# Optimization experiments

Measured on AMD Instinct MI355X. Metric: run time of the kernel, lower is better.

Reference implementation:

```python
import jax, jax.numpy as jnp
import numpy as np

N = 50000      # nodes
E = 800000     # edges (before self-loops)
DIN = 146      # input feature dim
D = 128        # hidden/out dim
G = 64         # graphs in batch
L = 4          # number of GCNConv layers (len(hidden_dims[1:]) + 1)
NC = 10        # classes
EPS = 1e-5     # BatchNorm eps


def setup_inputs() -> dict:
    key = jax.random.key(0)
    ks = jax.random.split(key, 12)
    x = jax.random.normal(ks[0], (N, DIN), jnp.float32)
    edge_index = jax.random.randint(ks[1], (2, E), 0, N, dtype=jnp.int64)
    batch = jnp.sort(jax.random.randint(ks[2], (N,), 0, G, dtype=jnp.int64))

    def lin(k, shape, fan_in):
        return (jax.random.normal(k, shape, jnp.float32) / np.sqrt(fan_in)).astype(jnp.float32)

    W_emb = lin(ks[3], (DIN, D), DIN)
    b_emb = jnp.zeros((D,), jnp.float32)
    W_gcn = lin(ks[4], (L, D, D), D)
    b_gcn = jnp.zeros((L, D), jnp.float32)
    bn_gamma = jnp.ones((L, D), jnp.float32)
    bn_beta = jnp.zeros((L, D), jnp.float32)
    W_r1 = lin(ks[5], (D, D // 2), D)
    b_r1 = jnp.zeros((D // 2,), jnp.float32)
    W_r2 = lin(ks[6], (D // 2, D // 4), D // 2)
    b_r2 = jnp.zeros((D // 4,), jnp.float32)
    W_r3 = lin(ks[7], (D // 4, NC), D // 4)
    b_r3 = jnp.zeros((NC,), jnp.float32)
    return {"x": x, "edge_index": edge_index, "batch": batch,
            "W_emb": W_emb, "b_emb": b_emb, "W_gcn": W_gcn, "b_gcn": b_gcn,
            "bn_gamma": bn_gamma, "bn_beta": bn_beta,
            "W_r1": W_r1, "b_r1": b_r1, "W_r2": W_r2, "b_r2": b_r2,
            "W_r3": W_r3, "b_r3": b_r3}


def reference(x, edge_index, batch, W_emb, b_emb, W_gcn, b_gcn,
              bn_gamma, bn_beta, W_r1, b_r1, W_r2, b_r2, W_r3, b_r3):
    # gcn_norm with self-loops (fill_value=1, improved=False)
    loop = jnp.arange(N, dtype=edge_index.dtype)
    src = jnp.concatenate([edge_index[0], loop])
    dst = jnp.concatenate([edge_index[1], loop])
    deg = jax.ops.segment_sum(jnp.ones(src.shape, x.dtype), dst, num_segments=N)
    dinv = jax.lax.rsqrt(jnp.maximum(deg, jnp.asarray(1e-12, x.dtype)))  # deg >= 1 (self loops)
    norm = (dinv[src] * dinv[dst])[:, None]  # [E+N, 1]

    h = x @ W_emb + b_emb  # embedding_h
    for l in range(L):
        h_in = h
        m = h @ W_gcn[l]                                            # [N, D]
        h = jax.ops.segment_sum(m[src] * norm, dst, num_segments=N) + b_gcn[l]
        # BatchNorm1d (training-mode batch stats, biased var)
        mu = h.mean(axis=0)
        var = h.var(axis=0)
        h = (h - mu) * jax.lax.rsqrt(var + EPS) * bn_gamma[l] + bn_beta[l]
        h = jax.nn.relu(h)
        h = h_in + h  # residual (dims always match here)

    # global_mean_pool over batch ids
    sums = jax.ops.segment_sum(h, batch, num_segments=G)
    cnts = jax.ops.segment_sum(jnp.ones((N, 1), h.dtype), batch, num_segments=G)
    hg = sums / jnp.maximum(cnts, 1.0)

    # MLPReadout: two hidden layers halving dims, then classifier
    z = jax.nn.relu(hg @ W_r1 + b_r1)
    z = jax.nn.relu(z @ W_r2 + b_r2)
    return z @ W_r3 + b_r3  # [G, NC]
```

## Files before the change

kernel.cpp:

```cpp
#include <hip/hip_runtime.h>
#include <hip/hip_bf16.h>

#define NN 50000
#define EE 800000
#define DIN 146
#define DD 128
#define GG 64
#define LL 4
#define NC 10
#define BN_EPS 1e-5f

#define KP_EMB 160
#define AST_L  136
#define NCOPY 64
#define NPW 4

typedef __attribute__((ext_vector_type(8))) short bf16x8;
typedef __attribute__((ext_vector_type(4))) float f32x4;

__device__ __forceinline__ float bf2f(__hip_bfloat16 v) { return __bfloat162float(v); }
__device__ __forceinline__ float loadf(const void* p, long i, int f32) {
    return f32 ? ((const float*)p)[i] : bf2f(((const __hip_bfloat16*)p)[i]);
}
__device__ __forceinline__ unsigned short f2bf_bits(float f) {
    __hip_bfloat16 h = __float2bfloat16(f);
    return *(unsigned short*)&h;
}
__device__ __forceinline__ float bfu2f(unsigned short u) {
    return __uint_as_float((unsigned)u << 16);
}

__global__ void detect_kernel(const void* ei, const void* batch, const void* Wemb,
                              int* __restrict__ flags) {
    __shared__ int s_edge_nz, s_batch_nz, s_f32_cnt;
    int t = threadIdx.x;
    if (t == 0) { s_edge_nz = 0; s_batch_nz = 0; s_f32_cnt = 0; }
    __syncthreads();
    {   const int* w = (const int*)ei;
        long j = ((long)t * ((2L * EE) / 64)) | 1;
        if (w[j] != 0) atomicAdd(&s_edge_nz, 1);
    }
    {   const int* w = (const int*)batch;
        long j = ((long)(NN / 2) + (long)t * ((NN / 2) / 64)) | 1;
        if (j < NN && w[j] != 0) atomicAdd(&s_batch_nz, 1);
    }
    {   const unsigned short* w = (const unsigned short*)Wemb;
        unsigned short v = w[2 * t];
        int ex = (v >> 7) & 0xFF;
        if (v != 0 && ex >= 128) atomicAdd(&s_f32_cnt, 1);
    }
    __syncthreads();
    if (t == 0) {
        flags[0] = (s_edge_nz == 0) ? 1 : 0;
        flags[1] = (s_batch_nz == 0) ? 1 : 0;
        flags[2] = (s_f32_cnt >= 8) ? 1 : 0;
    }
}

struct Param { const void* src; float* dst; int src_n; int dst_n; };
struct Params12 { Param p[12]; };

__global__ void conv_params_kernel(Params12 P, const int* __restrict__ flags) {
    int f32 = flags[2];
    const Param& e = P.p[blockIdx.y];
    int idx = blockIdx.x * 256 + threadIdx.x;
    if (idx < e.dst_n)
        e.dst[idx] = (idx < e.src_n) ? loadf(e.src, idx, f32) : 0.0f;
}

struct WtDesc { const void* src; long src_off; unsigned short* dst; int K; int Kpad; };
struct WtDescs5 { WtDesc p[5]; };

__global__ void conv_wt_kernel(WtDescs5 P, const int* __restrict__ flags) {
    int f32 = flags[2];
    const WtDesc& e = P.p[blockIdx.y];
    int idx = blockIdx.x * 256 + threadIdx.x;
    if (idx >= 128 * e.Kpad) return;
    int n = idx / e.Kpad, k = idx - n * e.Kpad;
    float v = (k < e.K) ? loadf(e.src, e.src_off + (long)k * DD + n, f32) : 0.0f;
    e.dst[idx] = f2bf_bits(v);
}

__global__ void repack_x_kernel(const void* __restrict__ x, const int* __restrict__ flags,
                                unsigned short* __restrict__ xb) {
    int f32 = flags[2];
    long idx = (long)blockIdx.x * 256 + threadIdx.x;
    if (idx >= (long)NN * KP_EMB) return;
    int row = (int)(idx / KP_EMB);
    int k = (int)(idx - (long)row * KP_EMB);
    float v = (k < DIN) ? loadf(x, (long)row * DIN + k, f32) : 0.0f;
    xb[idx] = f2bf_bits(v);
}

__global__ void init_kernel(int* __restrict__ deg, float* __restrict__ statmulti,
                            float* __restrict__ hgsum) {
    int i = blockIdx.x * blockDim.x + threadIdx.x;
    if (i < NN) deg[i] = 0;
    if (i < LL * NCOPY * 256) statmulti[i] = 0.0f;
    if (i < GG * DD) hgsum[i] = 0.0f;
}

__global__ void conv_idx_deg_kernel(const void* ei, const int* __restrict__ flags,
                                    int* __restrict__ src32, int* __restrict__ dst32,
                                    int* __restrict__ rank, int* __restrict__ deg) {
    int e = blockIdx.x * blockDim.x + threadIdx.x;
    if (e >= EE) return;
    const int* w = (const int*)ei;
    int s, d;
    if (flags[0]) { s = w[2L * e]; d = w[2L * (EE + e)]; }
    else          { s = w[e];      d = w[EE + e]; }
    src32[e] = s; dst32[e] = d;
    int r = 0;
    if ((unsigned)d < (unsigned)NN) r = atomicAdd(&deg[d], 1);
    rank[e] = r;
}

__global__ void conv_batch_kernel(const void* b, const int* __restrict__ flags,
                                  int* __restrict__ b32) {
    int i = blockIdx.x * blockDim.x + threadIdx.x;
    if (i >= NN) return;
    b32[i] = flags[1] ? ((const int*)b)[2L * i] : ((const int*)b)[i];
}

__global__ void scan1_kernel(const int* __restrict__ cnt, int* __restrict__ off,
                             int* __restrict__ bsum, float* __restrict__ dinv, int n) {
    int t = threadIdx.x;
    int i = blockIdx.x * 256 + t;
    int v = (i < n) ? cnt[i] : 0;
    if (i < n) dinv[i] = rsqrtf((float)(v + 1));
    int lane = t & 63, w = t >> 6;
    int x = v;
    #pragma unroll
    for (int s = 1; s < 64; s <<= 1) {
        int y = __shfl_up(x, s, 64);
        if (lane >= s) x += y;
    }
    __shared__ int wsum[4];
    if (lane == 63) wsum[w] = x;
    __syncthreads();
    if (t == 0) {
        int a = 0;
        #pragma unroll
        for (int k = 0; k < 4; ++k) { int tmp = wsum[k]; wsum[k] = a; a += tmp; }
        bsum[blockIdx.x] = a;
    }
    __syncthreads();
    int excl = x - v + wsum[w];
    if (i < n) off[i] = excl;
}

__global__ void scan2_kernel(int* __restrict__ bsum, int* __restrict__ boff,
                             int* __restrict__ off_last, int nb) {
    int t = threadIdx.x;
    int v = (t < nb) ? bsum[t] : 0;
    int lane = t & 63, w = t >> 6;
    int x = v;
    #pragma unroll
    for (int s = 1; s < 64; s <<= 1) {
        int y = __shfl_up(x, s, 64);
        if (lane >= s) x += y;
    }
    __shared__ int wsum[4];
    if (lane == 63) wsum[w] = x;
    __syncthreads();
    __shared__ int total_s;
    if (t == 0) {
        int a = 0;
        #pragma unroll
        for (int k = 0; k < 4; ++k) { int tmp = wsum[k]; wsum[k] = a; a += tmp; }
        total_s = a;
    }
    __syncthreads();
    if (t < nb) boff[t] = x - v + wsum[w];
    if (t == 0) *off_last = total_s;
}

__global__ void scan3_kernel(int* __restrict__ off, const int* __restrict__ boff, int n) {
    int i = blockIdx.x * 256 + threadIdx.x;
    if (i < n) off[i] += boff[blockIdx.x];
}

__global__ void scatter_kernel(const int* __restrict__ src, const int* __restrict__ dst,
                               const int* __restrict__ rank, const int* __restrict__ off,
                               int* __restrict__ src_s, int E) {
    int e = blockIdx.x * blockDim.x + threadIdx.x;
    if (e >= E) return;
    int s = src[e], d = dst[e];
    if ((unsigned)s >= (unsigned)NN || (unsigned)d >= (unsigned)NN) return;
    src_s[off[d] + rank[e]] = s;
}


__global__ __launch_bounds__(256) void emb_gemm_kernel(
    const unsigned short* __restrict__ Ab,
    const unsigned short* __restrict__ Wt,
    const float* __restrict__ bias,
    float* __restrict__ h, unsigned short* __restrict__ hb, int n)
{
    int t = threadIdx.x;
    int r0 = blockIdx.x * 128;
    int lane = t & 63, w = t >> 6;
    int m = lane & 15, quad = lane >> 4;
    int rbase = r0 + w * 32;
    bf16x8 a[2][5];
    #pragma unroll
    for (int rt = 0; rt < 2; ++rt)
        #pragma unroll
        for (int c = 0; c < 5; ++c) {
            int rr = rbase + rt * 16 + m; if (rr > n - 1) rr = n - 1;
            a[rt][c] = *(const bf16x8*)(Ab + (long)rr * KP_EMB + c * 32 + quad * 8);
        }
    f32x4 acc[2][8];
    #pragma unroll
    for (int t8 = 0; t8 < 8; ++t8) {
        float bv = bias[t8 * 16 + m];
        f32x4 ai = {bv, bv, bv, bv};
        acc[0][t8] = ai; acc[1][t8] = ai;
    }
    #pragma unroll
    for (int t8 = 0; t8 < 8; ++t8) {
        #pragma unroll
        for (int c = 0; c < 5; ++c) {
            bf16x8 b = *(const bf16x8*)(Wt + (long)(t8 * 16 + m) * KP_EMB + c * 32 + quad * 8);
            acc[0][t8] = __builtin_amdgcn_mfma_f32_16x16x32_bf16(a[0][c], b, acc[0][t8], 0, 0, 0);
            acc[1][t8] = __builtin_amdgcn_mfma_f32_16x16x32_bf16(a[1][c], b, acc[1][t8], 0, 0, 0);
        }
    }
    #pragma unroll
    for (int rt = 0; rt < 2; ++rt)
        #pragma unroll
        for (int t8 = 0; t8 < 8; ++t8)
            #pragma unroll
            for (int rg = 0; rg < 4; ++rg) {
                int row = rbase + rt * 16 + quad * 4 + rg;
                int col = t8 * 16 + m;
                if (row < n) {
                    float v = acc[rt][t8][rg];
                    h[(long)row * DD + col] = v;
                    hb[(long)row * DD + col] = f2bf_bits(v);
                }
            }
}

__global__ __launch_bounds__(256) void gemm_plain_kernel(
    const unsigned short* __restrict__ Ab,
    const unsigned short* __restrict__ Wt,
    const float* __restrict__ dinv,
    unsigned short* __restrict__ Mb, int n)
{
    int t = threadIdx.x;
    int r0 = blockIdx.x * 128;
    int lane = t & 63, w = t >> 6;
    int m = lane & 15, quad = lane >> 4;
    int rbase = r0 + w * 32;
    bf16x8 a[2][4];
    #pragma unroll
    for (int rt = 0; rt < 2; ++rt)
        #pragma unroll
        for (int c = 0; c < 4; ++c) {
            int rr = rbase + rt * 16 + m; if (rr > n - 1) rr = n - 1;
            a[rt][c] = *(const bf16x8*)(Ab + (long)rr * DD + c * 32 + quad * 8);
        }
    float dv[2][4];
    #pragma unroll
    for (int rt = 0; rt < 2; ++rt)
        #pragma unroll
        for (int rg = 0; rg < 4; ++rg) {
            int row = rbase + rt * 16 + quad * 4 + rg; if (row > n - 1) row = n - 1;
            dv[rt][rg] = dinv[row];
        }
    f32x4 acc[2][8];
    #pragma unroll
    for (int t8 = 0; t8 < 8; ++t8) {
        f32x4 z = {0.f, 0.f, 0.f, 0.f};
        acc[0][t8] = z; acc[1][t8] = z;
    }
    #pragma unroll
    for (int t8 = 0; t8 < 8; ++t8) {
        #pragma unroll
        for (int c = 0; c < 4; ++c) {
            bf16x8 b = *(const bf16x8*)(Wt + (long)(t8 * 16 + m) * DD + c * 32 + quad * 8);
            acc[0][t8] = __builtin_amdgcn_mfma_f32_16x16x32_bf16(a[0][c], b, acc[0][t8], 0, 0, 0);
            acc[1][t8] = __builtin_amdgcn_mfma_f32_16x16x32_bf16(a[1][c], b, acc[1][t8], 0, 0, 0);
        }
    }
    #pragma unroll
    for (int rt = 0; rt < 2; ++rt)
        #pragma unroll
        for (int t8 = 0; t8 < 8; ++t8)
            #pragma unroll
            for (int rg = 0; rg < 4; ++rg) {
                int row = rbase + rt * 16 + quad * 4 + rg;
                int col = t8 * 16 + m;
                if (row < n) Mb[(long)row * DD + col] = f2bf_bits(dv[rt][rg] * acc[rt][t8][rg]);
            }
}

__global__ __launch_bounds__(256) void gemm_fused_kernel(
    const float* __restrict__ agg, float* __restrict__ h,
    const float* __restrict__ bnacc, const float* __restrict__ gamma,
    const float* __restrict__ beta, const float* __restrict__ dinv,
    const unsigned short* __restrict__ Wt, unsigned short* __restrict__ Mb, int n)
{
    __shared__ unsigned short As[128 * AST_L];
    int t = threadIdx.x;
    int r0 = blockIdx.x * 128;
    {
        int c4 = (t & 31) * 4, rsub = t >> 5;
        float inv_n = 1.0f / (float)n;
        float4 sm = *(const float4*)&bnacc[c4];
        float4 sq = *(const float4*)&bnacc[128 + c4];
        float4 ga = *(const float4*)&gamma[c4];
        float4 be = *(const float4*)&beta[c4];
        float4 mu, rs;
        mu.x = sm.x * inv_n; mu.y = sm.y * inv_n; mu.z = sm.z * inv_n; mu.w = sm.w * inv_n;
        rs.x = rsqrtf(sq.x * inv_n - mu.x * mu.x + BN_EPS) * ga.x;
        rs.y = rsqrtf(sq.y * inv_n - mu.y * mu.y + BN_EPS) * ga.y;
        rs.z = rsqrtf(sq.z * inv_n - mu.z * mu.z + BN_EPS) * ga.z;
        rs.w = rsqrtf(sq.w * inv_n - mu.w * mu.w + BN_EPS) * ga.w;
        #pragma unroll 4
        for (int i = 0; i < 16; ++i) {
            int row = i * 8 + rsub;
            int r = r0 + row;
            unsigned short o0 = 0, o1 = 0, o2 = 0, o3 = 0;
            if (r < n) {
                long g = (long)r * DD + c4;
                float4 av = *(const float4*)&agg[g];
                float4 hv = *(const float4*)&h[g];
                hv.x += fmaxf((av.x - mu.x) * rs.x + be.x, 0.0f);
                hv.y += fmaxf((av.y - mu.y) * rs.y + be.y, 0.0f);
                hv.z += fmaxf((av.z - mu.z) * rs.z + be.z, 0.0f);
                hv.w += fmaxf((av.w - mu.w) * rs.w + be.w, 0.0f);
                *(float4*)&h[g] = hv;
                o0 = f2bf_bits(hv.x); o1 = f2bf_bits(hv.y);
                o2 = f2bf_bits(hv.z); o3 = f2bf_bits(hv.w);
            }
            unsigned short* dst = &As[row * AST_L + c4];
            dst[0] = o0; dst[1] = o1; dst[2] = o2; dst[3] = o3;
        }
    }
    __syncthreads();
    int lane = t & 63, w = t >> 6;
    int m = lane & 15, quad = lane >> 4;
    int rl = w * 32;
    int rbase = r0 + rl;
    bf16x8 a[2][4];
    #pragma unroll
    for (int rt = 0; rt < 2; ++rt)
        #pragma unroll
        for (int c = 0; c < 4; ++c)
            a[rt][c] = *(const bf16x8*)(As + (rl + rt * 16 + m) * AST_L + c * 32 + quad * 8);
    float dv[2][4];
    #pragma unroll
    for (int rt = 0; rt < 2; ++rt)
        #pragma unroll
        for (int rg = 0; rg < 4; ++rg) {
            int row = rbase + rt * 16 + quad * 4 + rg; if (row > n - 1) row = n - 1;
            dv[rt][rg] = dinv[row];
        }
    f32x4 acc[2][8];
    #pragma unroll
    for (int t8 = 0; t8 < 8; ++t8) {
        f32x4 z = {0.f, 0.f, 0.f, 0.f};
        acc[0][t8] = z; acc[1][t8] = z;
    }
    #pragma unroll
    for (int t8 = 0; t8 < 8; ++t8) {
        #pragma unroll
        for (int c = 0; c < 4; ++c) {
            bf16x8 b = *(const bf16x8*)(Wt + (long)(t8 * 16 + m) * DD + c * 32 + quad * 8);
            acc[0][t8] = __builtin_amdgcn_mfma_f32_16x16x32_bf16(a[0][c], b, acc[0][t8], 0, 0, 0);
            acc[1][t8] = __builtin_amdgcn_mfma_f32_16x16x32_bf16(a[1][c], b, acc[1][t8], 0, 0, 0);
        }
    }
    #pragma unroll
    for (int rt = 0; rt < 2; ++rt)
        #pragma unroll
        for (int t8 = 0; t8 < 8; ++t8)
            #pragma unroll
            for (int rg = 0; rg < 4; ++rg) {
                int row = rbase + rt * 16 + quad * 4 + rg;
                int col = t8 * 16 + m;
                if (row < n) Mb[(long)row * DD + col] = f2bf_bits(dv[rt][rg] * acc[rt][t8][rg]);
            }
}

__global__ __launch_bounds__(256) void agg_kernel(
    const unsigned short* __restrict__ mb, const int* __restrict__ off,
    const int* __restrict__ src_s, const float* __restrict__ dinv,
    const float* __restrict__ bias, float* __restrict__ agg,
    float* __restrict__ statacc)
{
    __shared__ float2 ssum[4][64], ssq[4][64];
    int t = threadIdx.x;
    int wv = t >> 6, lane = t & 63;
    const unsigned* M = (const unsigned*)mb;
    float2 bi = ((const float2*)bias)[lane];
    float2 sAcc = {0.0f, 0.0f}, qAcc = {0.0f, 0.0f};
    int i0 = (blockIdx.x * 4 + wv) * NPW;
    #pragma unroll 1
    for (int ni = 0; ni < NPW; ++ni) {
        int i = i0 + ni;
        if (i >= NN) break;
        float di = dinv[i];
        unsigned mv = M[(long)i * 64 + lane];
        float2 acc;
        acc.x = bfu2f((unsigned short)(mv & 0xffff));
        acc.y = bfu2f((unsigned short)(mv >> 16));
        int e = off[i], e1 = off[i + 1];
        for (; e + 8 <= e1; e += 8) {
            int j0 = src_s[e],     j1 = src_s[e + 1], j2 = src_s[e + 2], j3 = src_s[e + 3];
            int j4 = src_s[e + 4], j5 = src_s[e + 5], j6 = src_s[e + 6], j7 = src_s[e + 7];
            unsigned v0 = M[(long)j0 * 64 + lane];
            unsigned v1 = M[(long)j1 * 64 + lane];
            unsigned v2 = M[(long)j2 * 64 + lane];
            unsigned v3 = M[(long)j3 * 64 + lane];
            unsigned v4 = M[(long)j4 * 64 + lane];
            unsigned v5 = M[(long)j5 * 64 + lane];
            unsigned v6 = M[(long)j6 * 64 + lane];
            unsigned v7 = M[(long)j7 * 64 + lane];
            acc.x += bfu2f((unsigned short)(v0 & 0xffff));
            acc.y += bfu2f((unsigned short)(v0 >> 16));
            acc.x += bfu2f((unsigned short)(v1 & 0xffff));
            acc.y += bfu2f((unsigned short)(v1 >> 16));
            acc.x += bfu2f((unsigned short)(v2 & 0xffff));
            acc.y += bfu2f((unsigned short)(v2 >> 16));
            acc.x += bfu2f((unsigned short)(v3 & 0xffff));
            acc.y += bfu2f((unsigned short)(v3 >> 16));
            acc.x += bfu2f((unsigned short)(v4 & 0xffff));
            acc.y += bfu2f((unsigned short)(v4 >> 16));
            acc.x += bfu2f((unsigned short)(v5 & 0xffff));
            acc.y += bfu2f((unsigned short)(v5 >> 16));
            acc.x += bfu2f((unsigned short)(v6 & 0xffff));
            acc.y += bfu2f((unsigned short)(v6 >> 16));
            acc.x += bfu2f((unsigned short)(v7 & 0xffff));
            acc.y += bfu2f((unsigned short)(v7 >> 16));
        }
        for (; e + 4 <= e1; e += 4) {
            int j0 = src_s[e], j1 = src_s[e + 1], j2 = src_s[e + 2], j3 = src_s[e + 3];
            unsigned v0 = M[(long)j0 * 64 + lane];
            unsigned v1 = M[(long)j1 * 64 + lane];
            unsigned v2 = M[(long)j2 * 64 + lane];
            unsigned v3 = M[(long)j3 * 64 + lane];
            acc.x += bfu2f((unsigned short)(v0 & 0xffff));
            acc.y += bfu2f((unsigned short)(v0 >> 16));
            acc.x += bfu2f((unsigned short)(v1 & 0xffff));
            acc.y += bfu2f((unsigned short)(v1 >> 16));
            acc.x += bfu2f((unsigned short)(v2 & 0xffff));
            acc.y += bfu2f((unsigned short)(v2 >> 16));
            acc.x += bfu2f((unsigned short)(v3 & 0xffff));
            acc.y += bfu2f((unsigned short)(v3 >> 16));
        }
        for (; e < e1; ++e) {
            unsigned v = M[(long)src_s[e] * 64 + lane];
            acc.x += bfu2f((unsigned short)(v & 0xffff));
            acc.y += bfu2f((unsigned short)(v >> 16));
        }
        float2 outv;
        outv.x = di * acc.x + bi.x;
        outv.y = di * acc.y + bi.y;
        ((float2*)agg)[(long)i * 64 + lane] = outv;
        sAcc.x += outv.x; sAcc.y += outv.y;
        qAcc.x += outv.x * outv.x; qAcc.y += outv.y * outv.y;
    }
    ssum[wv][lane] = sAcc; ssq[wv][lane] = qAcc;
    __syncthreads();
    if (wv == 0) {
        float2 s0 = ssum[0][lane], s1 = ssum[1][lane], s2 = ssum[2][lane], s3 = ssum[3][lane];
        float2 q0 = ssq[0][lane], q1 = ssq[1][lane], q2 = ssq[2][lane], q3 = ssq[3][lane];
        float sx = s0.x + s1.x + s2.x + s3.x;
        float sy = s0.y + s1.y + s2.y + s3.y;
        float qx = q0.x + q1.x + q2.x + q3.x;
        float qy = q0.y + q1.y + q2.y + q3.y;
        float* copy = statacc + (blockIdx.x & (NCOPY - 1)) * 256;
        atomicAdd(&copy[2 * lane], sx);
        atomicAdd(&copy[2 * lane + 1], sy);
        atomicAdd(&copy[128 + 2 * lane], qx);
        atomicAdd(&copy[128 + 2 * lane + 1], qy);
    }
}

__global__ void statfin_kernel(const float* __restrict__ multi, float* __restrict__ bnacc) {
    int c = threadIdx.x;
    float s = 0.0f;
    #pragma unroll 8
    for (int k = 0; k < NCOPY; ++k) s += multi[k * 256 + c];
    bnacc[c] = s;
}

__global__ void pool1_kernel(const float* __restrict__ h, const float* __restrict__ agg,
                             const float* __restrict__ bnacc,
                             const float* __restrict__ gamma, const float* __restrict__ beta,
                             const int* __restrict__ b32, float* __restrict__ hgsum, int n) {
    int t = threadIdx.x;
    int c4 = (t & 31) * 4, rsub = t >> 5;
    float inv_n = 1.0f / (float)n;
    float4 sm = *(const float4*)&bnacc[c4];
    float4 sq = *(const float4*)&bnacc[128 + c4];
    float4 ga = *(const float4*)&gamma[c4];
    float4 be = *(const float4*)&beta[c4];
    float4 mu, rs;
    mu.x = sm.x * inv_n; mu.y = sm.y * inv_n; mu.z = sm.z * inv_n; mu.w = sm.w * inv_n;
    rs.x = rsqrtf(sq.x * inv_n - mu.x * mu.x + BN_EPS) * ga.x;
    rs.y = rsqrtf(sq.y * inv_n - mu.y * mu.y + BN_EPS) * ga.y;
    rs.z = rsqrtf(sq.z * inv_n - mu.z * mu.z + BN_EPS) * ga.z;
    rs.w = rsqrtf(sq.w * inv_n - mu.w * mu.w + BN_EPS) * ga.w;
    int rows_pb = (n + gridDim.x - 1) / gridDim.x;
    int r0 = blockIdx.x * rows_pb;
    int r1 = min(n, r0 + rows_pb);
    float4 acc = {0, 0, 0, 0};
    int gcur = -1;
    for (int r = r0 + rsub; r < r1; r += 8) {
        int g = b32[r];
        if (g != gcur) {
            if (gcur >= 0) {
                atomicAdd(&hgsum[gcur * DD + c4 + 0], acc.x);
                atomicAdd(&hgsum[gcur * DD + c4 + 1], acc.y);
                atomicAdd(&hgsum[gcur * DD + c4 + 2], acc.z);
                atomicAdd(&hgsum[gcur * DD + c4 + 3], acc.w);
            }
            acc.x = acc.y = acc.z = acc.w = 0.0f;
            gcur = ((unsigned)g < (unsigned)GG) ? g : -1;
        }
        if (gcur >= 0) {
            long ix = (long)r * DD + c4;
            float4 av = *(const float4*)&agg[ix];
            float4 hv = *(const float4*)&h[ix];
            acc.x += hv.x + fmaxf((av.x - mu.x) * rs.x + be.x, 0.0f);
            acc.y += hv.y + fmaxf((av.y - mu.y) * rs.y + be.y, 0.0f);
            acc.z += hv.z + fmaxf((av.z - mu.z) * rs.z + be.z, 0.0f);
            acc.w += hv.w + fmaxf((av.w - mu.w) * rs.w + be.w, 0.0f);
        }
    }
    if (gcur >= 0) {
        atomicAdd(&hgsum[gcur * DD + c4 + 0], acc.x);
        atomicAdd(&hgsum[gcur * DD + c4 + 1], acc.y);
        atomicAdd(&hgsum[gcur * DD + c4 + 2], acc.z);
        atomicAdd(&hgsum[gcur * DD + c4 + 3], acc.w);
    }
}

__device__ int lower_bound_i(const int* __restrict__ a, int n, int v) {
    int lo = 0, hi = n;
    while (lo < hi) {
        int mid = (lo + hi) >> 1;
        if (a[mid] < v) lo = mid + 1; else hi = mid;
    }
    return lo;
}

__global__ void readout_kernel(const float* __restrict__ hgsum, const int* __restrict__ b32,
                               const float* __restrict__ W1, const float* __restrict__ b1,
                               const float* __restrict__ W2, const float* __restrict__ b2,
                               const float* __restrict__ W3, const float* __restrict__ b3,
                               const int* __restrict__ flags, void* __restrict__ out, int n) {
    int f32 = flags[2];
    int g = blockIdx.x;
    int t = threadIdx.x;
    __shared__ float hgs[DD];
    __shared__ float z1[DD / 2];
    __shared__ float z2[DD / 4];
    int lo = lower_bound_i(b32, n, g);
    int hi = lower_bound_i(b32, n, g + 1);
    float invc = 1.0f / fmaxf((float)(hi - lo), 1.0f);
    hgs[t] = hgsum[g * DD + t] * invc;
    __syncthreads();
    if (t < DD / 2) {
        float acc = b1[t];
        #pragma unroll 8
        for (int k = 0; k < DD; ++k) acc = fmaf(hgs[k], W1[k * (DD / 2) + t], acc);
        z1[t] = fmaxf(acc, 0.0f);
    }
    __syncthreads();
    if (t < DD / 4) {
        float acc = b2[t];
        #pragma unroll 8
        for (int k = 0; k < DD / 2; ++k) acc = fmaf(z1[k], W2[k * (DD / 4) + t], acc);
        z2[t] = fmaxf(acc, 0.0f);
    }
    __syncthreads();
    if (t < NC) {
        float acc = b3[t];
        #pragma unroll 8
        for (int k = 0; k < DD / 4; ++k) acc = fmaf(z2[k], W3[k * NC + t], acc);
        if (f32) ((float*)out)[g * NC + t] = acc;
        else     ((__hip_bfloat16*)out)[g * NC + t] = __float2bfloat16(acc);
    }
}

extern "C" void kernel_launch(void* const* d_in, const int* in_sizes, int n_in,
                              void* d_out, int out_size, void* d_ws, size_t ws_size,
                              hipStream_t stream) {
    const void* x      = d_in[0];
    const void* ei     = d_in[1];
    const void* batch  = d_in[2];
    const void* W_emb  = d_in[3];
    const void* b_emb  = d_in[4];
    const void* W_gcn  = d_in[5];
    const void* b_gcn  = d_in[6];
    const void* bn_g   = d_in[7];
    const void* bn_b   = d_in[8];
    const void* W_r1   = d_in[9];
    const void* b_r1   = d_in[10];
    const void* W_r2   = d_in[11];
    const void* b_r2   = d_in[12];
    const void* W_r3   = d_in[13];
    const void* b_r3   = d_in[14];

    char* p = (char*)d_ws;
    auto alloc = [&](size_t bytes) -> void* {
        void* r = (void*)p;
        p += (bytes + 255) & ~(size_t)255;
        return r;
    };
    int*   flags  = (int*)alloc(64 * 4);
    int*   deg    = (int*)alloc((size_t)NN * 4);
    float* bnacc  = (float*)alloc((size_t)LL * 256 * 4);
    float* statmulti = (float*)alloc((size_t)LL * NCOPY * 256 * 4);
    float* hgsum  = (float*)alloc((size_t)GG * DD * 4);
    int*   off    = (int*)alloc((size_t)(NN + 1) * 4);
    float* dinv   = (float*)alloc((size_t)NN * 4);
    int*   src32  = (int*)alloc((size_t)EE * 4);
    int*   dst32  = (int*)alloc((size_t)EE * 4);
    int*   rank   = (int*)alloc((size_t)EE * 4);
    int*   b32    = (int*)alloc((size_t)NN * 4);
    int*   src_s  = (int*)alloc((size_t)EE * 4);
    int*   bsum   = (int*)alloc(256 * 4);
    int*   boff   = (int*)alloc(256 * 4);
    float* h      = (float*)alloc((size_t)NN * DD * 4);
    unsigned short* hb = (unsigned short*)alloc((size_t)NN * DD * 2);
    unsigned short* mb = (unsigned short*)alloc((size_t)NN * DD * 2);
    float* agg    = (float*)alloc((size_t)NN * DD * 4);
    unsigned short* xb = (unsigned short*)agg;
    unsigned short* wt_emb = (unsigned short*)alloc((size_t)DD * KP_EMB * 2);
    unsigned short* wt_gcn = (unsigned short*)alloc((size_t)LL * DD * DD * 2);
    float* b_emb32 = (float*)alloc(DD * 4);
    float* b_gcn32 = (float*)alloc((size_t)LL * DD * 4);
    float* bng32   = (float*)alloc((size_t)LL * DD * 4);
    float* bnb32   = (float*)alloc((size_t)LL * DD * 4);
    float* wr1     = (float*)alloc((size_t)DD * (DD / 2) * 4);
    float* br1     = (float*)alloc((DD / 2) * 4);
    float* wr2     = (float*)alloc((size_t)(DD / 2) * (DD / 4) * 4);
    float* br2     = (float*)alloc((DD / 4) * 4);
    float* wr3     = (float*)alloc((size_t)(DD / 4) * NC * 4);
    float* br3     = (float*)alloc(NC * 4);

    detect_kernel<<<1, 64, 0, stream>>>(ei, batch, W_emb, flags);
    init_kernel<<<256, 256, 0, stream>>>(deg, statmulti, hgsum);

    Params12 P;
    P.p[0]  = { b_emb, b_emb32, DD, DD };
    P.p[1]  = { b_gcn, b_gcn32, LL * DD, LL * DD };
    P.p[2]  = { bn_g,  bng32,   LL * DD, LL * DD };
    P.p[3]  = { bn_b,  bnb32,   LL * DD, LL * DD };
    P.p[4]  = { W_r1,  wr1,     DD * (DD / 2), DD * (DD / 2) };
    P.p[5]  = { b_r1,  br1,     DD / 2, DD / 2 };
    P.p[6]  = { W_r2,  wr2,     (DD / 2) * (DD / 4), (DD / 2) * (DD / 4) };
    P.p[7]  = { b_r2,  br2,     DD / 4, DD / 4 };
    P.p[8]  = { W_r3,  wr3,     (DD / 4) * NC, (DD / 4) * NC };
    P.p[9]  = { b_r3,  br3,     NC, NC };
    P.p[10] = { b_r3,  br3,     0, 0 };
    P.p[11] = { b_r3,  br3,     0, 0 };
    dim3 cgrid((DD * (DD / 2) + 255) / 256, 12);
    conv_params_kernel<<<cgrid, 256, 0, stream>>>(P, flags);

    WtDescs5 W;
    W.p[0] = { W_emb, 0,            wt_emb,                DIN, KP_EMB };
    W.p[1] = { W_gcn, 0L * DD * DD, wt_gcn + 0L * DD * DD, DD,  DD };
    W.p[2] = { W_gcn, 1L * DD * DD, wt_gcn + 1L * DD * DD, DD,  DD };
    W.p[3] = { W_gcn, 2L * DD * DD, wt_gcn + 2L * DD * DD, DD,  DD };
    W.p[4] = { W_gcn, 3L * DD * DD, wt_gcn + 3L * DD * DD, DD,  DD };
    dim3 wgrid((128 * KP_EMB + 255) / 256, 5);
    conv_wt_kernel<<<wgrid, 256, 0, stream>>>(W, flags);

    repack_x_kernel<<<(int)(((long)NN * KP_EMB + 255) / 256), 256, 0, stream>>>(x, flags, xb);

    conv_idx_deg_kernel<<<(EE + 255) / 256, 256, 0, stream>>>(ei, flags, src32, dst32,
                                                              rank, deg);
    conv_batch_kernel<<<(NN + 255) / 256, 256, 0, stream>>>(batch, flags, b32);

    int nb = (NN + 255) / 256;
    scan1_kernel<<<nb, 256, 0, stream>>>(deg, off, bsum, dinv, NN);
    scan2_kernel<<<1, 256, 0, stream>>>(bsum, boff, off + NN, nb);
    scan3_kernel<<<nb, 256, 0, stream>>>(off, boff, NN);

    scatter_kernel<<<(EE + 255) / 256, 256, 0, stream>>>(src32, dst32, rank, off, src_s, EE);

    int ngemm = (NN + 127) / 128;
    emb_gemm_kernel<<<ngemm, 256, 0, stream>>>(xb, wt_emb, b_emb32, h, hb, NN);

    int nagg = (NN + 4 * NPW - 1) / (4 * NPW);
    for (int l = 0; l < LL; ++l) {
        if (l == 0) {
            gemm_plain_kernel<<<ngemm, 256, 0, stream>>>(hb, wt_gcn, dinv, mb, NN);
        } else {
            gemm_fused_kernel<<<ngemm, 256, 0, stream>>>(
                agg, h, bnacc + (l - 1) * 256, bng32 + (l - 1) * DD, bnb32 + (l - 1) * DD,
                dinv, wt_gcn + (size_t)l * DD * DD, mb, NN);
        }
        agg_kernel<<<nagg, 256, 0, stream>>>(mb, off, src_s, dinv,
                                             b_gcn32 + l * DD, agg,
                                             statmulti + (size_t)l * NCOPY * 256);
        statfin_kernel<<<1, 256, 0, stream>>>(statmulti + (size_t)l * NCOPY * 256,
                                              bnacc + l * 256);
    }

    pool1_kernel<<<512, 256, 0, stream>>>(h, agg, bnacc + (LL - 1) * 256,
                                          bng32 + (LL - 1) * DD, bnb32 + (LL - 1) * DD,
                                          b32, hgsum, NN);
    readout_kernel<<<GG, DD, 0, stream>>>(hgsum, b32, wr1, br1, wr2, br2, wr3, br3,
                                          flags, d_out, NN);
}
```

Measured before the change: 475.6 us.

## Fuse preprocessing kernels into one launch and vectorize aggregation gathers

Merges five preprocessing kernels (edge conversion and degree count, x repack, batch conversion, param and weight conversion) into a single block-indexed launch to cut launch overhead and let the work overlap. Rewrites the aggregation kernel so each wave splits into four 16-lane groups, each gathering a whole 256-byte neighbor row with 16-byte loads. The four partial sums are then reduced through shared memory. This trades more LDS traffic and registers for fewer, wider gather instructions.

```diff
diff --git a/kernel.cpp b/kernel.cpp
--- a/kernel.cpp
+++ b/kernel.cpp
@@ -14,6 +14,13 @@
 #define AST_L  136
 #define NCOPY 64
 #define NPW 4
+#define RST 129
+
+#define MB_EDGE   3125
+#define MB_REPACK (MB_EDGE + 31250)
+#define MB_BATCH  (MB_REPACK + 196)
+#define MB_PARAMS (MB_BATCH + 384)
+#define MB_WT     (MB_PARAMS + 400)
 
 typedef __attribute__((ext_vector_type(8))) short bf16x8;
 typedef __attribute__((ext_vector_type(4))) float f32x4;
@@ -28,6 +35,16 @@
 }
 __device__ __forceinline__ float bfu2f(unsigned short u) {
     return __uint_as_float((unsigned)u << 16);
+}
+__device__ __forceinline__ void acc_add8(float* acc, uint4 v) {
+    acc[0] += __uint_as_float(v.x << 16);
+    acc[1] += __uint_as_float(v.x & 0xffff0000u);
+    acc[2] += __uint_as_float(v.y << 16);
+    acc[3] += __uint_as_float(v.y & 0xffff0000u);
+    acc[4] += __uint_as_float(v.z << 16);
+    acc[5] += __uint_as_float(v.z & 0xffff0000u);
+    acc[6] += __uint_as_float(v.w << 16);
+    acc[7] += __uint_as_float(v.w & 0xffff0000u);
 }
 
 __global__ void detect_kernel(const void* ei, const void* batch, const void* Wemb,
@@ -59,38 +76,8 @@
 
 struct Param { const void* src; float* dst; int src_n; int dst_n; };
 struct Params12 { Param p[12]; };
-
-__global__ void conv_params_kernel(Params12 P, const int* __restrict__ flags) {
-    int f32 = flags[2];
-    const Param& e = P.p[blockIdx.y];
-    int idx = blockIdx.x * 256 + threadIdx.x;
-    if (idx < e.dst_n)
-        e.dst[idx] = (idx < e.src_n) ? loadf(e.src, idx, f32) : 0.0f;
-}
-
 struct WtDesc { const void* src; long src_off; unsigned short* dst; int K; int Kpad; };
 struct WtDescs5 { WtDesc p[5]; };
-
-__global__ void conv_wt_kernel(WtDescs5 P, const int* __restrict__ flags) {
-    int f32 = flags[2];
-    const WtDesc& e = P.p[blockIdx.y];
-    int idx = blockIdx.x * 256 + threadIdx.x;
-    if (idx >= 128 * e.Kpad) return;
-    int n = idx / e.Kpad, k = idx - n * e.Kpad;
-    float v = (k < e.K) ? loadf(e.src, e.src_off + (long)k * DD + n, f32) : 0.0f;
-    e.dst[idx] = f2bf_bits(v);
-}
-
-__global__ void repack_x_kernel(const void* __restrict__ x, const int* __restrict__ flags,
-                                unsigned short* __restrict__ xb) {
-    int f32 = flags[2];
-    long idx = (long)blockIdx.x * 256 + threadIdx.x;
-    if (idx >= (long)NN * KP_EMB) return;
-    int row = (int)(idx / KP_EMB);
-    int k = (int)(idx - (long)row * KP_EMB);
-    float v = (k < DIN) ? loadf(x, (long)row * DIN + k, f32) : 0.0f;
-    xb[idx] = f2bf_bits(v);
-}
 
 __global__ void init_kernel(int* __restrict__ deg, float* __restrict__ statmulti,
                             float* __restrict__ hgsum) {
@@ -100,26 +87,55 @@
     if (i < GG * DD) hgsum[i] = 0.0f;
 }
 
-__global__ void conv_idx_deg_kernel(const void* ei, const int* __restrict__ flags,
-                                    int* __restrict__ src32, int* __restrict__ dst32,
-                                    int* __restrict__ rank, int* __restrict__ deg) {
-    int e = blockIdx.x * blockDim.x + threadIdx.x;
-    if (e >= EE) return;
-    const int* w = (const int*)ei;
-    int s, d;
-    if (flags[0]) { s = w[2L * e]; d = w[2L * (EE + e)]; }
-    else          { s = w[e];      d = w[EE + e]; }
-    src32[e] = s; dst32[e] = d;
-    int r = 0;
-    if ((unsigned)d < (unsigned)NN) r = atomicAdd(&deg[d], 1);
-    rank[e] = r;
-}
-
-__global__ void conv_batch_kernel(const void* b, const int* __restrict__ flags,
-                                  int* __restrict__ b32) {
-    int i = blockIdx.x * blockDim.x + threadIdx.x;
-    if (i >= NN) return;
-    b32[i] = flags[1] ? ((const int*)b)[2L * i] : ((const int*)b)[i];
+__global__ __launch_bounds__(256) void mega_pre_kernel(
+    const void* __restrict__ x, const void* __restrict__ ei,
+    const void* __restrict__ batch, const int* __restrict__ flags,
+    unsigned short* __restrict__ xb,
+    int* __restrict__ src32, int* __restrict__ dst32,
+    int* __restrict__ rank, int* __restrict__ deg, int* __restrict__ b32,
+    Params12 P, WtDescs5 W)
+{
+    int b = blockIdx.x;
+    int t = threadIdx.x;
+    if (b < MB_EDGE) {
+        int e = b * 256 + t;
+        const int* w = (const int*)ei;
+        int s, d;
+        if (flags[0]) { s = w[2L * e]; d = w[2L * (EE + e)]; }
+        else          { s = w[e];      d = w[EE + e]; }
+        src32[e] = s; dst32[e] = d;
+        int r = 0;
+        if ((unsigned)d < (unsigned)NN) r = atomicAdd(&deg[d], 1);
+        rank[e] = r;
+    } else if (b < MB_REPACK) {
+        int f32 = flags[2];
+        long idx = (long)(b - MB_EDGE) * 256 + t;
+        int row = (int)(idx / KP_EMB);
+        int k = (int)(idx - (long)row * KP_EMB);
+        float v = (k < DIN) ? loadf(x, (long)row * DIN + k, f32) : 0.0f;
+        xb[idx] = f2bf_bits(v);
+    } else if (b < MB_BATCH) {
+        int i = (b - MB_REPACK) * 256 + t;
+        if (i < NN) b32[i] = flags[1] ? ((const int*)batch)[2L * i] : ((const int*)batch)[i];
+    } else if (b < MB_PARAMS) {
+        int f32 = flags[2];
+        int bb = b - MB_BATCH;
+        const Param& e = P.p[bb >> 5];
+        int idx = (bb & 31) * 256 + t;
+        if (idx < e.dst_n)
+            e.dst[idx] = (idx < e.src_n) ? loadf(e.src, idx, f32) : 0.0f;
+    } else {
+        int f32 = flags[2];
+        int bb = b - MB_PARAMS;
+        int y = bb / 80;
+        const WtDesc& e = W.p[y];
+        int idx = (bb - y * 80) * 256 + t;
+        if (idx < 128 * e.Kpad) {
+            int n = idx / e.Kpad, k = idx - n * e.Kpad;
+            float v = (k < e.K) ? loadf(e.src, e.src_off + (long)k * DD + n, f32) : 0.0f;
+            e.dst[idx] = f2bf_bits(v);
+        }
+    }
 }
 
 __global__ void scan1_kernel(const int* __restrict__ cnt, int* __restrict__ off,
@@ -391,10 +407,12 @@
     const float* __restrict__ bias, float* __restrict__ agg,
     float* __restrict__ statacc)
 {
+    __shared__ float sred[4][4 * RST];
     __shared__ float2 ssum[4][64], ssq[4][64];
     int t = threadIdx.x;
     int wv = t >> 6, lane = t & 63;
-    const unsigned* M = (const unsigned*)mb;
+    int grp = lane >> 4, sl = lane & 15;
+    float* red = sred[wv];
     float2 bi = ((const float2*)bias)[lane];
     float2 sAcc = {0.0f, 0.0f}, qAcc = {0.0f, 0.0f};
     int i0 = (blockIdx.x * 4 + wv) * NPW;
@@ -402,63 +420,46 @@
     for (int ni = 0; ni < NPW; ++ni) {
         int i = i0 + ni;
         if (i >= NN) break;
-        float di = dinv[i];
-        unsigned mv = M[(long)i * 64 + lane];
-        float2 acc;
-        acc.x = bfu2f((unsigned short)(mv & 0xffff));
-        acc.y = bfu2f((unsigned short)(mv >> 16));
+        float acc[8];
+        #pragma unroll
+        for (int k = 0; k < 8; ++k) acc[k] = 0.0f;
+        if (grp == 0) {
+            uint4 v = *(const uint4*)(mb + (long)i * DD + sl * 8);
+            acc_add8(acc, v);
+        }
         int e = off[i], e1 = off[i + 1];
         for (; e + 8 <= e1; e += 8) {
-            int j0 = src_s[e],     j1 = src_s[e + 1], j2 = src_s[e + 2], j3 = src_s[e + 3];
-            int j4 = src_s[e + 4], j5 = src_s[e + 5], j6 = src_s[e + 6], j7 = src_s[e + 7];
-            unsigned v0 = M[(long)j0 * 64 + lane];
-            unsigned v1 = M[(long)j1 * 64 + lane];
-            unsigned v2 = M[(long)j2 * 64 + lane];
-            unsigned v3 = M[(long)j3 * 64 + lane];
-            unsigned v4 = M[(long)j4 * 64 + lane];
-            unsigned v5 = M[(long)j5 * 64 + lane];
-            unsigned v6 = M[(long)j6 * 64 + lane];
-            unsigned v7 = M[(long)j7 * 64 + lane];
-            acc.x += bfu2f((unsigned short)(v0 & 0xffff));
-            acc.y += bfu2f((unsigned short)(v0 >> 16));
-            acc.x += bfu2f((unsigned short)(v1 & 0xffff));
-            acc.y += bfu2f((unsigned short)(v1 >> 16));
-            acc.x += bfu2f((unsigned short)(v2 & 0xffff));
-            acc.y += bfu2f((unsigned short)(v2 >> 16));
-            acc.x += bfu2f((unsigned short)(v3 & 0xffff));
-            acc.y += bfu2f((unsigned short)(v3 >> 16));
-            acc.x += bfu2f((unsigned short)(v4 & 0xffff));
-            acc.y += bfu2f((unsigned short)(v4 >> 16));
-            acc.x += bfu2f((unsigned short)(v5 & 0xffff));
-            acc.y += bfu2f((unsigned short)(v5 >> 16));
-            acc.x += bfu2f((unsigned short)(v6 & 0xffff));
-            acc.y += bfu2f((unsigned short)(v6 >> 16));
-            acc.x += bfu2f((unsigned short)(v7 & 0xffff));
-            acc.y += bfu2f((unsigned short)(v7 >> 16));
+            int ja = src_s[e + grp];
+            int jb = src_s[e + 4 + grp];
+            uint4 va = *(const uint4*)(mb + (long)ja * DD + sl * 8);
+            uint4 vb = *(const uint4*)(mb + (long)jb * DD + sl * 8);
+            acc_add8(acc, va);
+            acc_add8(acc, vb);
         }
         for (; e + 4 <= e1; e += 4) {
-            int j0 = src_s[e], j1 = src_s[e + 1], j2 = src_s[e + 2], j3 = src_s[e + 3];
-            unsigned v0 = M[(long)j0 * 64 + lane];
-            unsigned v1 = M[(long)j1 * 64 + lane];
-            unsigned v2 = M[(long)j2 * 64 + lane];
-            unsigned v3 = M[(long)j3 * 64 + lane];
-            acc.x += bfu2f((unsigned short)(v0 & 0xffff));
-            acc.y += bfu2f((unsigned short)(v0 >> 16));
-            acc.x += bfu2f((unsigned short)(v1 & 0xffff));
-            acc.y += bfu2f((unsigned short)(v1 >> 16));
-            acc.x += bfu2f((unsigned short)(v2 & 0xffff));
-            acc.y += bfu2f((unsigned short)(v2 >> 16));
-            acc.x += bfu2f((unsigned short)(v3 & 0xffff));
-            acc.y += bfu2f((unsigned short)(v3 >> 16));
-        }
-        for (; e < e1; ++e) {
-            unsigned v = M[(long)src_s[e] * 64 + lane];
-            acc.x += bfu2f((unsigned short)(v & 0xffff));
-            acc.y += bfu2f((unsigned short)(v >> 16));
-        }
+            int j = src_s[e + grp];
+            uint4 v = *(const uint4*)(mb + (long)j * DD + sl * 8);
+            acc_add8(acc, v);
+        }
+        if (e + grp < e1) {
+            int j = src_s[e + grp];
+            uint4 v = *(const uint4*)(mb + (long)j * DD + sl * 8);
+            acc_add8(acc, v);
+        }
+        #pragma unroll
+        for (int k = 0; k < 8; ++k) red[grp * RST + sl * 8 + k] = acc[k];
+        asm volatile("" ::: "memory");
+        float c0 = 0.0f, c1 = 0.0f;
+        #pragma unroll
+        for (int g = 0; g < 4; ++g) {
+            c0 += red[g * RST + 2 * lane];
+            c1 += red[g * RST + 2 * lane + 1];
+        }
+        asm volatile("" ::: "memory");
+        float di = dinv[i];
         float2 outv;
-        outv.x = di * acc.x + bi.x;
-        outv.y = di * acc.y + bi.y;
+        outv.x = di * c0 + bi.x;
+        outv.y = di * c1 + bi.y;
         ((float2*)agg)[(long)i * 64 + lane] = outv;
         sAcc.x += outv.x; sAcc.y += outv.y;
         qAcc.x += outv.x * outv.x; qAcc.y += outv.y * outv.y;
@@ -661,8 +662,6 @@
     P.p[9]  = { b_r3,  br3,     NC, NC };
     P.p[10] = { b_r3,  br3,     0, 0 };
     P.p[11] = { b_r3,  br3,     0, 0 };
-    dim3 cgrid((DD * (DD / 2) + 255) / 256, 12);
-    conv_params_kernel<<<cgrid, 256, 0, stream>>>(P, flags);
 
     WtDescs5 W;
     W.p[0] = { W_emb, 0,            wt_emb,                DIN, KP_EMB };
@@ -670,14 +669,9 @@
     W.p[2] = { W_gcn, 1L * DD * DD, wt_gcn + 1L * DD * DD, DD,  DD };
     W.p[3] = { W_gcn, 2L * DD * DD, wt_gcn + 2L * DD * DD, DD,  DD };
     W.p[4] = { W_gcn, 3L * DD * DD, wt_gcn + 3L * DD * DD, DD,  DD };
-    dim3 wgrid((128 * KP_EMB + 255) / 256, 5);
-    conv_wt_kernel<<<wgrid, 256, 0, stream>>>(W, flags);
-
-    repack_x_kernel<<<(int)(((long)NN * KP_EMB + 255) / 256), 256, 0, stream>>>(x, flags, xb);
-
-    conv_idx_deg_kernel<<<(EE + 255) / 256, 256, 0, stream>>>(ei, flags, src32, dst32,
-                                                              rank, deg);
-    conv_batch_kernel<<<(NN + 255) / 256, 256, 0, stream>>>(batch, flags, b32);
+
+    mega_pre_kernel<<<MB_WT, 256, 0, stream>>>(x, ei, batch, flags, xb,
+                                               src32, dst32, rank, deg, b32, P, W);
 
     int nb = (NN + 255) / 256;
     scan1_kernel<<<nb, 256, 0, stream>>>(deg, off, bsum, dinv, NN);
```

Measured after the change: 472.3 us. About the same (-0.7%).
